# Optimization experiments

Hardware: AMD Instinct MI355X
Metric: run time of the kernel (lower is better)

Reference implementation:

```python
import jax, jax.numpy as jnp
import numpy as np
from jax import lax

B, C, HW = 256, 3, 128
OC, K = 16, 3
NH, FANIN, NO = 256, 512, 10
F = OC * 63 * 63  # 63504 flattened features after conv(k=3,valid)->pool(2)


def setup_inputs() -> dict:
    key = jax.random.key(0)
    ks = jax.random.split(key, 8)
    inputs = jax.random.normal(ks[0], (B, C, HW, HW), dtype=jnp.float32)
    conv_w = jax.random.normal(ks[1], (OC, C, K, K), dtype=jnp.float32) * 0.1
    conv_b = jax.random.normal(ks[2], (OC,), dtype=jnp.float32) * 0.1
    hidden_idx = jax.random.randint(ks[3], (NH, FANIN), 0, F, dtype=jnp.int64 if jax.config.jax_enable_x64 else jnp.int32)
    hidden_w = jax.random.normal(ks[4], (NH, FANIN), dtype=jnp.float32) * (1.0 / np.sqrt(FANIN))
    hidden_b = jax.random.normal(ks[5], (NH,), dtype=jnp.float32) * 0.1
    out_w = jax.random.normal(ks[6], (NO, NH), dtype=jnp.float32) * (1.0 / np.sqrt(NH))
    out_b = jax.random.normal(ks[7], (NO,), dtype=jnp.float32) * 0.1
    return {"inputs": inputs, "conv_w": conv_w, "conv_b": conv_b,
            "hidden_idx": hidden_idx, "hidden_w": hidden_w, "hidden_b": hidden_b,
            "out_w": out_w, "out_b": out_b}


def reference(inputs, conv_w, conv_b, hidden_idx, hidden_w, hidden_b, out_w, out_b):
    # --- feature extraction: conv(valid) -> relu -> maxpool(2) -> flatten ---
    x = lax.conv_general_dilated(inputs, conv_w, window_strides=(1, 1), padding='VALID',
                                 dimension_numbers=('NCHW', 'OIHW', 'NCHW'))
    x = jax.nn.relu(x + conv_b[None, :, None, None])            # [B, OC, 126, 126]
    x = lax.reduce_window(x, -jnp.inf, lax.max,
                          window_dimensions=(1, 1, 2, 2),
                          window_strides=(1, 1, 2, 2), padding='VALID')  # [B, OC, 63, 63]
    feats = x.reshape(x.shape[0], -1)                           # [B, F] (row-major == torch.flatten)
    # --- NEAT-style classification: per-node gather -> tiny linear -> sigmoid ---
    gathered = feats[:, hidden_idx]                             # [B, NH, FANIN] irregular gather
    hidden = jax.nn.sigmoid(jnp.einsum('bhk,hk->bh', gathered, hidden_w) + hidden_b)  # [B, NH]
    out = jax.nn.sigmoid(hidden @ out_w.T + out_b)              # [B, NO]
    return out
```

## Files before the change

kernel.cpp:

```cpp
#include <hip/hip_runtime.h>
#include <hip/hip_fp16.h>
#include <math.h>

#define BATCH 256
#define CIN 3
#define HW 128
#define OC 16
#define POOLED 63
#define FEAT 63504
#define NH 256
#define FANIN 512
#define NO 10

#define PADX 134
#define ROWS 12

typedef _Float16 h4 __attribute__((ext_vector_type(4)));
typedef _Float16 h2v __attribute__((ext_vector_type(2)));
typedef float    f4 __attribute__((ext_vector_type(4)));

__global__ __launch_bounds__(256) void conv_pool_kernel(const float* __restrict__ inp,
                                                        const float* __restrict__ cw,
                                                        const float* __restrict__ cb,
                                                        __half* __restrict__ featsT) {
    __shared__ _Float16 sB[ROWS * 16 * PADX];
    const int t    = threadIdx.x;
    const int l    = t & 63;
    const int w    = t >> 6;
    const int q    = l >> 4;
    const int bcol = l & 15;

    const int id = blockIdx.x;
    const int u  = id & 7;
    const int v  = id >> 3;
    const int i  = v >> 1;
    const int g  = 2 * u + (v & 1);
    const int y0 = 2 * i;

#pragma unroll
    for (int bb = 0; bb < 4; ++bb) {
        const int b_l = w * 4 + bb;
#pragma unroll
        for (int rr = 0; rr < 12; ++rr) {
            const int c  = rr >> 2;
            const int dy = rr & 3;
            const float2 vv = *(const float2*)
                &inp[((size_t)(g * 16 + b_l) * CIN + c) * (HW * HW) + (y0 + dy) * HW + 2 * l];
            *(__half2*)&sB[(size_t)((c * 4 + dy) * 16 + b_l) * PADX + 2 * l] =
                __float22half2_rn(vv);
        }
    }
    __syncthreads();

    h4  aF[3][2];
    int bOff[3][2];
    float bias[4];
#pragma unroll
    for (int s = 0; s < 3; ++s) {
        const int rIdx = s * 4 + q;
        const int c    = (rIdx * 11) >> 5;
        const int ky   = rIdx - 3 * c;
        const bool valid = (c < 3);
        float wv[3];
#pragma unroll
        for (int kx = 0; kx < 3; ++kx)
            wv[kx] = valid ? cw[(bcol * CIN + c) * 9 + ky * 3 + kx] : 0.0f;
        aF[s][0][0] = (_Float16)wv[0]; aF[s][0][1] = (_Float16)wv[1];
        aF[s][0][2] = (_Float16)wv[2]; aF[s][0][3] = (_Float16)0.0f;
        aF[s][1][0] = (_Float16)0.0f;  aF[s][1][1] = (_Float16)wv[0];
        aF[s][1][2] = (_Float16)wv[1]; aF[s][1][3] = (_Float16)wv[2];
#pragma unroll
        for (int ys = 0; ys < 2; ++ys) {
            const int row = valid ? (c * 4 + ys + ky) : ys;
            bOff[s][ys] = (row * 16 + bcol) * PADX;
        }
    }
#pragma unroll
    for (int r = 0; r < 4; ++r) bias[r] = cb[4 * q + r];

    const int jend = (16 * w + 16 < 63) ? (16 * w + 16) : 63;
    for (int j = 16 * w; j < jend; ++j) {
        f4 d00 = {0.f,0.f,0.f,0.f}, d01 = d00, d10 = d00, d11 = d00;
#pragma unroll
        for (int s = 0; s < 3; ++s) {
            const _Float16* p0 = &sB[bOff[s][0] + 2 * j];
            const _Float16* p1 = &sB[bOff[s][1] + 2 * j];
            const h2v a0 = *(const h2v*)p0, a1 = *(const h2v*)(p0 + 2);
            const h2v c0 = *(const h2v*)p1, c1 = *(const h2v*)(p1 + 2);
            const h4 bF0 = {a0[0], a0[1], a1[0], a1[1]};
            const h4 bF1 = {c0[0], c0[1], c1[0], c1[1]};
            d00 = __builtin_amdgcn_mfma_f32_16x16x16f16(aF[s][0], bF0, d00, 0, 0, 0);
            d01 = __builtin_amdgcn_mfma_f32_16x16x16f16(aF[s][1], bF0, d01, 0, 0, 0);
            d10 = __builtin_amdgcn_mfma_f32_16x16x16f16(aF[s][0], bF1, d10, 0, 0, 0);
            d11 = __builtin_amdgcn_mfma_f32_16x16x16f16(aF[s][1], bF1, d11, 0, 0, 0);
        }
#pragma unroll
        for (int r = 0; r < 4; ++r) {
            const float mv = fmaxf(fmaxf(d00[r], d01[r]), fmaxf(d10[r], d11[r]));
            const float rv = fmaxf(mv + bias[r], 0.0f);
            const int oc = 4 * q + r;
            const __half hv = __float2half_rn(rv);
            __builtin_nontemporal_store(
                *(const short*)&hv,
                (short*)&featsT[(size_t)(oc * 3969 + i * POOLED + j) * BATCH + g * 16 + bcol]);
        }
    }
}

__global__ __launch_bounds__(256) void hidden_kernel(const __half* __restrict__ featsT,
                                                     const int* __restrict__ hidx,
                                                     const float* __restrict__ hw,
                                                     float* __restrict__ hiddenP) {
    __shared__ int   sidx[128];
    __shared__ float swt[128];
    __shared__ float red[4][256];
    const int h = blockIdx.x;
    const int q = blockIdx.y;
    const int t = threadIdx.x;
    if (t < 128) {
        sidx[t] = hidx[h * FANIN + q * 128 + t];
        swt[t]  = hw[h * FANIN + q * 128 + t];
    }
    __syncthreads();

    const int l   = t & 63;
    const int w   = t >> 6;
    const int hl  = l & 31;
    const int sel = l >> 5;
    float acc[8] = {0.f,0.f,0.f,0.f,0.f,0.f,0.f,0.f};
#pragma unroll
    for (int m = 0; m < 16; ++m) {
        const int kloc = w * 32 + 2 * m + sel;
        const uint4 v = *(const uint4*)(featsT + (size_t)sidx[kloc] * BATCH + 8 * hl);
        const __half2* hp = reinterpret_cast<const __half2*>(&v);
        const float wt = swt[kloc];
#pragma unroll
        for (int d2 = 0; d2 < 4; ++d2) {
            const float2 f = __half22float2(hp[d2]);
            acc[2 * d2 + 0] += f.x * wt;
            acc[2 * d2 + 1] += f.y * wt;
        }
    }
#pragma unroll
    for (int e = 0; e < 8; ++e) acc[e] += __shfl_xor(acc[e], 32);
    if (sel == 0) {
#pragma unroll
        for (int e = 0; e < 8; ++e) red[w][8 * hl + e] = acc[e];
    }
    __syncthreads();

    if (t < 256) {
        const float s = red[0][t] + red[1][t] + red[2][t] + red[3][t];
        hiddenP[((size_t)q * NH + h) * BATCH + t] = s;
    }
}

__global__ __launch_bounds__(256) void out_kernel(const float* __restrict__ hiddenP,
                                                  const float* __restrict__ hb,
                                                  const float* __restrict__ ow,
                                                  const float* __restrict__ ob,
                                                  float* __restrict__ out) {
    __shared__ float red[256];
    const int o  = blockIdx.x;
    const int bt = blockIdx.y;
    const int tb = threadIdx.x & 15;
    const int hg = threadIdx.x >> 4;
    const int b  = bt * 16 + tb;
    float acc = 0.f;
#pragma unroll
    for (int k = 0; k < 16; ++k) {
        const int h = hg * 16 + k;
        const float s = hiddenP[(0 * NH + h) * BATCH + b]
                      + hiddenP[(1 * NH + h) * BATCH + b]
                      + hiddenP[(2 * NH + h) * BATCH + b]
                      + hiddenP[(3 * NH + h) * BATCH + b] + hb[h];
        const float hs = 1.0f / (1.0f + __expf(-s));
        acc += hs * ow[o * NH + h];
    }
    red[threadIdx.x] = acc;
    __syncthreads();
    if (hg == 0) {
        float s = 0.f;
#pragma unroll
        for (int gg = 0; gg < 16; ++gg) s += red[gg * 16 + tb];
        out[b * NO + o] = 1.0f / (1.0f + __expf(-(s + ob[o])));
    }
}

extern "C" void kernel_launch(void* const* d_in, const int* in_sizes, int n_in,
                              void* d_out, int out_size, void* d_ws, size_t ws_size,
                              hipStream_t stream) {
    const float* inputs   = (const float*)d_in[0];
    const float* conv_w   = (const float*)d_in[1];
    const float* conv_b   = (const float*)d_in[2];
    const int*   hidden_i = (const int*)d_in[3];
    const float* hidden_w = (const float*)d_in[4];
    const float* hidden_b = (const float*)d_in[5];
    const float* out_w    = (const float*)d_in[6];
    const float* out_b    = (const float*)d_in[7];
    float* out = (float*)d_out;

    char* ws = (char*)d_ws;
    __half* featsT  = (__half*)ws;
    float*  hiddenP = (float*)(ws + (size_t)FEAT * BATCH * 2);

    conv_pool_kernel<<<1008, 256, 0, stream>>>(inputs, conv_w, conv_b, featsT);
    hidden_kernel<<<dim3(NH, 4), 256, 0, stream>>>(featsT, hidden_i, hidden_w, hiddenP);
    out_kernel<<<dim3(NO, 16), 256, 0, stream>>>(hiddenP, hidden_b, out_w, out_b, out);
}
```

Before: 129.6 us.

## Split conv-pool blocks along width into halves to double grid parallelism

Each conv/pool block now covers half of the output columns (32 of 63) with a 70-wide shared tile plus a halo, and the grid doubles to 2016 blocks. Each wave handles 8 pooled columns instead of 16. The smaller shared-memory footprint should raise occupancy and spread the work across more CUs. The cost is reloading the overlapping halo columns, a generic strided load loop that uses a division, and halved per-block reuse.

```diff
diff --git a/kernel.cpp b/kernel.cpp
--- a/kernel.cpp
+++ b/kernel.cpp
@@ -12,8 +12,7 @@
 #define FANIN 512
 #define NO 10
 
-#define PADX 134
-#define ROWS 12
+#define PW 70
 
 typedef _Float16 h4 __attribute__((ext_vector_type(4)));
 typedef _Float16 h2v __attribute__((ext_vector_type(2)));
@@ -23,7 +22,7 @@
                                                         const float* __restrict__ cw,
                                                         const float* __restrict__ cb,
                                                         __half* __restrict__ featsT) {
-    __shared__ _Float16 sB[ROWS * 16 * PADX];
+    __shared__ _Float16 sB[192 * PW];
     const int t    = threadIdx.x;
     const int l    = t & 63;
     const int w    = t >> 6;
@@ -33,21 +32,25 @@
     const int id = blockIdx.x;
     const int u  = id & 7;
     const int v  = id >> 3;
-    const int i  = v >> 1;
-    const int g  = 2 * u + (v & 1);
+    const int jh = v & 1;
+    const int tt = v >> 1;
+    const int i  = tt >> 1;
+    const int g  = 2 * u + (tt & 1);
     const int y0 = 2 * i;
-
-#pragma unroll
-    for (int bb = 0; bb < 4; ++bb) {
-        const int b_l = w * 4 + bb;
-#pragma unroll
-        for (int rr = 0; rr < 12; ++rr) {
-            const int c  = rr >> 2;
-            const int dy = rr & 3;
+    const int xbase = 64 * jh;
+
+    for (int e = t; e < 192 * 35; e += 256) {
+        const int r  = e / 35;
+        const int xi = e - r * 35;
+        const int gx = xbase + 2 * xi;
+        if (gx <= 126) {
+            const int c4 = r >> 4;
+            const int bl = r & 15;
+            const int c  = c4 >> 2;
+            const int dy = c4 & 3;
             const float2 vv = *(const float2*)
-                &inp[((size_t)(g * 16 + b_l) * CIN + c) * (HW * HW) + (y0 + dy) * HW + 2 * l];
-            *(__half2*)&sB[(size_t)((c * 4 + dy) * 16 + b_l) * PADX + 2 * l] =
-                __float22half2_rn(vv);
+                &inp[((size_t)(g * 16 + bl) * CIN + c) * (HW * HW) + (y0 + dy) * HW + gx];
+            *(__half2*)&sB[(size_t)r * PW + (gx - xbase)] = __float22half2_rn(vv);
         }
     }
     __syncthreads();
@@ -72,19 +75,24 @@
 #pragma unroll
         for (int ys = 0; ys < 2; ++ys) {
             const int row = valid ? (c * 4 + ys + ky) : ys;
-            bOff[s][ys] = (row * 16 + bcol) * PADX;
+            bOff[s][ys] = (row * 16 + bcol) * PW;
         }
     }
 #pragma unroll
     for (int r = 0; r < 4; ++r) bias[r] = cb[4 * q + r];
 
-    const int jend = (16 * w + 16 < 63) ? (16 * w + 16) : 63;
-    for (int j = 16 * w; j < jend; ++j) {
+    const int jbeg = 32 * jh + 8 * w;
+#pragma unroll 1
+    for (int jl = 0; jl < 8; ++jl) {
+        const int j = jbeg + jl;
+        if (j > 62) break;
+        const int xl = 2 * j - xbase;
+
         f4 d00 = {0.f,0.f,0.f,0.f}, d01 = d00, d10 = d00, d11 = d00;
 #pragma unroll
         for (int s = 0; s < 3; ++s) {
-            const _Float16* p0 = &sB[bOff[s][0] + 2 * j];
-            const _Float16* p1 = &sB[bOff[s][1] + 2 * j];
+            const _Float16* p0 = &sB[bOff[s][0] + xl];
+            const _Float16* p1 = &sB[bOff[s][1] + xl];
             const h2v a0 = *(const h2v*)p0, a1 = *(const h2v*)(p0 + 2);
             const h2v c0 = *(const h2v*)p1, c1 = *(const h2v*)(p1 + 2);
             const h4 bF0 = {a0[0], a0[1], a1[0], a1[1]};
@@ -204,7 +212,7 @@
     __half* featsT  = (__half*)ws;
     float*  hiddenP = (float*)(ws + (size_t)FEAT * BATCH * 2);
 
-    conv_pool_kernel<<<1008, 256, 0, stream>>>(inputs, conv_w, conv_b, featsT);
+    conv_pool_kernel<<<2016, 256, 0, stream>>>(inputs, conv_w, conv_b, featsT);
     hidden_kernel<<<dim3(NH, 4), 256, 0, stream>>>(featsT, hidden_i, hidden_w, hiddenP);
     out_kernel<<<dim3(NO, 16), 256, 0, stream>>>(hiddenP, hidden_b, out_w, out_b, out);
 }
```

New measurement: 145.2 us. 1.12x slower.
